# Kernel optimization log

Measured on AMD Instinct MI355X. Metric: run time of the kernel, lower is better.

Reference implementation:

```python
import jax, jax.numpy as jnp
import numpy as np

VOCAB, EMB, HID, OUT = 1000, 256, 512, 1
NUM_IN, NUM_OUT = 7, 4
B, S = 64, 512
D = EMB + NUM_OUT  # conv input dim = 260


def setup_inputs() -> dict:
    key = jax.random.key(0)
    ks = jax.random.split(key, 8)
    ev = jax.random.randint(ks[0], (B, S, 1), 0, VOCAB).astype(jnp.float32)
    num = jax.random.normal(ks[1], (B, S, NUM_IN), jnp.float32)
    X = jnp.concatenate([ev, num], axis=-1)  # [B,S,8]; col 0 = event ids
    def w(k, shape, fan_in):
        return jax.random.normal(k, shape, jnp.float32) / np.sqrt(fan_in).astype(np.float32)
    return {
        "X": X,
        "emb": w(ks[2], (VOCAB, EMB), EMB),
        "Wn": w(ks[3], (NUM_IN, NUM_OUT), NUM_IN), "bn": jnp.zeros((NUM_OUT,), jnp.float32),
        "Wf": w(ks[4], (D, 3 * HID), D), "bf": jnp.zeros((3 * HID,), jnp.float32),
        "Wb": w(ks[5], (D, 3 * HID), D), "bb": jnp.zeros((3 * HID,), jnp.float32),
        "Wo": w(ks[6], (2 * HID, OUT), 2 * HID), "bo": jnp.zeros((OUT,), jnp.float32),
    }


def _fo_pool(Z, F):
    # Z, F: [S, B, H]. Linear recurrence h_t = F_t * h_{t-1} + (1 - F_t) * Z_t.
    def step(h, zf):
        z, f = zf
        h = f * h + (1.0 - f) * z
        return h, h
    h0 = jnp.zeros(Z.shape[1:], Z.dtype)
    _, hs = jax.lax.scan(step, h0, (Z, F))
    return hs  # [S, B, H]


def _forward(X, emb, Wn, bn, Wf, bf, Wb, bb, Wo, bo):
    ev = jax.lax.stop_gradient(X[:, :, 0]).astype(jnp.int32)  # event-type ids
    num = X[:, :, 1:]
    e = emb[ev]                          # [B,S,EMB]
    n = num @ Wn + bn                    # [B,S,NUM_OUT]
    c = jnp.concatenate([e, n], axis=-1)  # [B,S,D]

    def gates(W, b):
        g = jnp.einsum('bsd,dk->sbk', c, W) + b  # kernel-1 conv == GEMM; [S,B,3H]
        Z, F = g[..., :HID], g[..., HID:2 * HID]  # O gate is computed but unused upstream
        return jnp.tanh(Z), jax.nn.sigmoid(F)

    Zf, Ff = gates(Wf, bf)
    Zb, Fb = gates(Wb, bb)
    hf = _fo_pool(Zf, Ff)                       # forward direction
    hb = _fo_pool(Zb[::-1], Fb[::-1])[::-1]     # backward: scan reversed, re-reverse
    # torch takes h_combined[-1]: last forward state, first backward-scan state
    final = jnp.concatenate([hf[-1], hb[-1]], axis=-1)  # [B, 2H]
    return final @ Wo + bo  # dropout p=0 is identity


def reference(X, emb, Wn, bn, Wf, bf, Wb, bb, Wo, bo):
    return _forward(X, emb, Wn, bn, Wf, bf, Wb, bb, Wo, bo)
```

## Files before the change

kernel.cpp:

```cpp
#include <hip/hip_runtime.h>
#include <stdint.h>

#define B_ 64
#define S_ 512
#define EMB_ 256
#define NIN_ 7
#define NOUT_ 4
#define HID_ 512
#define VOCAB_ 1000
#define VP_ 1024
#define NG_ 2048

typedef __bf16 bf16x8 __attribute__((ext_vector_type(8)));
typedef float floatx4 __attribute__((ext_vector_type(4)));
typedef unsigned short u16x8 __attribute__((ext_vector_type(8)));
typedef unsigned long long ull;

__device__ __forceinline__ unsigned short f2bf(float f) {
    unsigned u = __float_as_uint(f);
    u += 0x7FFFu + ((u >> 16) & 1u);
    return (unsigned short)(u >> 16);
}
__device__ __forceinline__ float bf2f(unsigned short h) {
    return __uint_as_float(((unsigned)h) << 16);
}
__device__ __forceinline__ float rcp_(float x) { return __builtin_amdgcn_rcpf(x); }
__device__ __forceinline__ float exp2_(float x) {
    float r; asm("v_exp_f32 %0, %1" : "=v"(r) : "v"(x)); return r;
}
#define L2E_ 1.4426950408889634f
__device__ __forceinline__ float sigmoidf_(float x) {
    return rcp_(1.0f + exp2_(x * (-L2E_)));
}
__device__ __forceinline__ float tanhf_(float x) {
    float ax = fabsf(x);
    float e = exp2_(ax * (-2.0f * L2E_));
    float t = (1.0f - e) * rcp_(1.0f + e);
    return copysignf(t, x);
}


__global__ __launch_bounds__(256) void prep(
    const float* __restrict__ emb, const float* __restrict__ bn,
    const float* __restrict__ Wf, const float* __restrict__ bfv,
    const float* __restrict__ Wb, const float* __restrict__ bb,
    unsigned short* __restrict__ Aemb, unsigned short* __restrict__ WT,
    float* __restrict__ W4, float* __restrict__ bvec,
    unsigned* __restrict__ bcnt) {
    int bid = blockIdx.x;
    int tid = threadIdx.x;

    if (bid < 64) {
        int g = bid;
#pragma unroll
        for (int half = 0; half < 2; ++half) {
            int t = tid + 256 * half;
            int r15 = t & 15;
            int kchunk = (t >> 4) & 3;
            int kt = t >> 6;
            int row = g * 16 + r15;
            int k0 = kt * 32 + kchunk * 8;
            unsigned short p[8];
            if (row < VOCAB_) {
                float4 a = *(const float4*)(emb + (size_t)row * EMB_ + k0);
                float4 b = *(const float4*)(emb + (size_t)row * EMB_ + k0 + 4);
                p[0]=f2bf(a.x); p[1]=f2bf(a.y); p[2]=f2bf(a.z); p[3]=f2bf(a.w);
                p[4]=f2bf(b.x); p[5]=f2bf(b.y); p[6]=f2bf(b.z); p[7]=f2bf(b.w);
            } else {
#pragma unroll
                for (int q = 0; q < 8; ++q) p[q] = 0;
            }
            size_t chunk = ((size_t)(g >> 3) * 8 + kt) * 8 + (g & 7);
            *(u16x8*)(Aemb + chunk * 512 + (16 * kchunk + r15) * 8) =
                *(const u16x8*)p;
        }
    } else if (bid < 192) {
        __shared__ float raw[32][132];
        int job = bid - 64;
        int idx = job >> 3;
        int kt  = job & 7;
        int p = idx >> 3;
        int gq = idx & 7;
        const float* W = p ? Wb : Wf;
        int j0 = gq * 64;
        int r = tid >> 3;
        int i = tid & 7;
        int k0 = kt * 32;

        const float* src = W + (size_t)(k0 + r) * 1536;
        float4 a0 = *(const float4*)(src + j0 + i * 8);
        float4 a1 = *(const float4*)(src + j0 + i * 8 + 4);
        float4 b0 = *(const float4*)(src + 512 + j0 + i * 8);
        float4 b1 = *(const float4*)(src + 512 + j0 + i * 8 + 4);
        *(float4*)&raw[r][i * 8]          = a0;
        *(float4*)&raw[r][i * 8 + 4]      = a1;
        *(float4*)&raw[r][64 + i * 8]     = b0;
        *(float4*)&raw[r][64 + i * 8 + 4] = b1;
        __syncthreads();
#pragma unroll
        for (int h = 0; h < 2; ++h) {
            int e = tid + 256 * h;
            int gl = e >> 6;
            int rest = e & 63;
            int kchunk = rest >> 4;
            int v15 = rest & 15;
            int joff = gl * 8 + (v15 >> 1);
            int cl = joff + 64 * (v15 & 1);
            unsigned short pk[8];
#pragma unroll
            for (int q = 0; q < 8; ++q) pk[q] = f2bf(raw[kchunk * 8 + q][cl]);
            int g = p * 64 + gq * 8 + gl;
            size_t chunk = ((size_t)(g >> 3) * 8 + kt) * 8 + (g & 7);
            *(u16x8*)(WT + chunk * 512 + (16 * kchunk + v15) * 8) =
                *(const u16x8*)pk;
        }
    } else {
        int v = (bid - 192) * 256 + tid;
        int part = v >> 10;
        int m = v & 1023;
        int j = m >> 1;
        int c = (m & 1) ? (512 + j) : j;
        const float* W = part ? Wb : Wf;
        float bv = part ? bb[c] : bfv[c];
#pragma unroll
        for (int q = 0; q < NOUT_; ++q) {
            float w = W[(size_t)(256 + q) * 1536 + c];
            W4[(size_t)q * NG_ + v] = w;
            bv = fmaf(bn[q], w, bv);
        }
        bvec[v] = bv;
        if (bid == 192 && tid < 64) bcnt[tid] = 0;
    }
}

__global__ __launch_bounds__(256) void gemmG(
    const float* __restrict__ X,
    const unsigned short* __restrict__ Aemb, const unsigned short* __restrict__ WT,
    const float* __restrict__ bvec,
    unsigned short* __restrict__ G1, unsigned short* __restrict__ Gb) {
    int bid = blockIdx.x;
    int tid = threadIdx.x;
    int lane = tid & 63, wave = tid >> 6;
    int rl = lane & 15;

    if (bid < 64) {
        int mtile = bid & 7;
        int ntile = bid >> 3;
        int r0 = mtile * 128;
        int n0 = ntile * 128;
        int wm = wave & 1, wn = wave >> 1;

        const unsigned short* pa = Aemb + ((size_t)mtile * 64 + 4 * wm) * 512 + lane * 8;
        const unsigned short* pb = WT + ((size_t)ntile * 64 + 4 * wn) * 512 + lane * 8;

        floatx4 acc[4][4];
#pragma unroll
        for (int mi = 0; mi < 4; ++mi)
#pragma unroll
            for (int ni = 0; ni < 4; ++ni) acc[mi][ni] = (floatx4){0.f, 0.f, 0.f, 0.f};

        bf16x8 afc[4], bfc[4], afn[4], bfn[4];
#pragma unroll
        for (int mi = 0; mi < 4; ++mi) afc[mi] = *(const bf16x8*)(pa + mi * 512);
#pragma unroll
        for (int ni = 0; ni < 4; ++ni) bfc[ni] = *(const bf16x8*)(pb + ni * 512);

#pragma unroll
        for (int kt = 0; kt < 8; ++kt) {
            if (kt < 7) {
#pragma unroll
                for (int mi = 0; mi < 4; ++mi)
                    afn[mi] = *(const bf16x8*)(pa + (size_t)(kt + 1) * 4096 + mi * 512);
#pragma unroll
                for (int ni = 0; ni < 4; ++ni)
                    bfn[ni] = *(const bf16x8*)(pb + (size_t)(kt + 1) * 4096 + ni * 512);
            }
#pragma unroll
            for (int mi = 0; mi < 4; ++mi)
#pragma unroll
                for (int ni = 0; ni < 4; ++ni)
                    acc[mi][ni] = __builtin_amdgcn_mfma_f32_16x16x32_bf16(afc[mi], bfc[ni], acc[mi][ni], 0, 0, 0);
            if (kt < 7) {
#pragma unroll
                for (int mi = 0; mi < 4; ++mi) afc[mi] = afn[mi];
#pragma unroll
                for (int ni = 0; ni < 4; ++ni) bfc[ni] = bfn[ni];
            }
        }

#pragma unroll
        for (int ni = 0; ni < 4; ++ni) {
            int n = n0 + 64 * wn + 16 * ni + rl;
            float bv = bvec[n];
#pragma unroll
            for (int mi = 0; mi < 4; ++mi) {
                int rb = r0 + 64 * wm + 16 * mi + (lane >> 4) * 4;
#pragma unroll
                for (int v = 0; v < 4; ++v)
                    G1[(size_t)(rb + v) * 1024 + n] = f2bf(acc[mi][ni][v] + bv);
            }
        }
    } else {
        __shared__ int evs[64];
        int ntile = bid - 64;
        int n0 = ntile * 128;
        if (tid < 64)
            evs[tid] = (int)X[((size_t)tid * S_ + (S_ - 1)) * 8];
        __syncthreads();

        int cbase[4];
#pragma unroll
        for (int mi = 0; mi < 4; ++mi) {
            int R = evs[16 * mi + rl];
            int g = R >> 4;
            cbase[mi] = (g >> 3) * 32768 + (g & 7) * 512 + (lane >> 4) * 128 + (R & 15) * 8;
        }
        const unsigned short* pb = WT + ((size_t)(8 + ntile) * 64 + 2 * wave) * 512 + lane * 8;

        floatx4 acc[4][2];
#pragma unroll
        for (int mi = 0; mi < 4; ++mi)
#pragma unroll
            for (int ni = 0; ni < 2; ++ni) acc[mi][ni] = (floatx4){0.f, 0.f, 0.f, 0.f};

#pragma unroll
        for (int kt = 0; kt < 8; ++kt) {
            bf16x8 afc[4], bfc[2];
#pragma unroll
            for (int mi = 0; mi < 4; ++mi)
                afc[mi] = *(const bf16x8*)(Aemb + (size_t)cbase[mi] + (size_t)kt * 4096);
#pragma unroll
            for (int ni = 0; ni < 2; ++ni)
                bfc[ni] = *(const bf16x8*)(pb + (size_t)kt * 4096 + ni * 512);
#pragma unroll
            for (int mi = 0; mi < 4; ++mi)
#pragma unroll
                for (int ni = 0; ni < 2; ++ni)
                    acc[mi][ni] = __builtin_amdgcn_mfma_f32_16x16x32_bf16(afc[mi], bfc[ni], acc[mi][ni], 0, 0, 0);
        }

#pragma unroll
        for (int ni = 0; ni < 2; ++ni) {
            int n = n0 + 32 * wave + 16 * ni + rl;
            float bv = bvec[1024 + n];
#pragma unroll
            for (int mi = 0; mi < 4; ++mi) {
                int rb = 16 * mi + (lane >> 4) * 4;
#pragma unroll
                for (int v = 0; v < 4; ++v)
                    Gb[(size_t)(rb + v) * 1024 + n] = f2bf(acc[mi][ni][v] + bv);
            }
        }
    }
}

__global__ __launch_bounds__(512, 4) void scanF(
    const float* __restrict__ X, const unsigned short* __restrict__ G1,
    const unsigned short* __restrict__ Gb, const float* __restrict__ W4,
    const float* __restrict__ Wn, const float* __restrict__ Wo,
    const float* __restrict__ bo, float* __restrict__ PQ,
    unsigned* __restrict__ bcnt, float* __restrict__ out) {
    __shared__ float LX[512];
    __shared__ float LN[64][4];
    __shared__ int   LO[64];
    __shared__ unsigned lastf;
    __shared__ float red[8];
    int bid = blockIdx.x;
    int b = bid >> 3, chunk = bid & 7;
    int s0 = chunk * 64;
    int j = threadIdx.x;

    LX[j] = X[((size_t)b * S_ + s0 + (j >> 3)) * 8 + (j & 7)];
    __syncthreads();

    if (j < 64) LO[j] = (int)LX[j * 8] * 2048;
    if (j < 256) {
        int t = j >> 2, q = j & 3;
        float s = 0.f;
#pragma unroll
        for (int i = 0; i < NIN_; ++i) s = fmaf(LX[t * 8 + 1 + i], Wn[i * NOUT_ + q], s);
        LN[t][q] = s;
    }

    float2 w4p[NOUT_];
#pragma unroll
    for (int q = 0; q < NOUT_; ++q)
        w4p[q] = *(const float2*)(W4 + (size_t)q * NG_ + 2 * j);
    __syncthreads();

    const char* Gbase = (const char*)G1 + 4 * j;
    unsigned gp[64];
#pragma unroll
    for (int m = 0; m < 16; ++m) {
        int4 lo = *(const int4*)&LO[4 * m];
        gp[4 * m + 0] = *(const unsigned*)(Gbase + lo.x);
        gp[4 * m + 1] = *(const unsigned*)(Gbase + lo.y);
        gp[4 * m + 2] = *(const unsigned*)(Gbase + lo.z);
        gp[4 * m + 3] = *(const unsigned*)(Gbase + lo.w);
    }

    float P = 1.f, Q = 0.f;
#pragma unroll
    for (int s = 0; s < 64; ++s) {
        unsigned gpc = gp[s];
        float gz = bf2f((unsigned short)(gpc & 0xffffu));
        float gf = bf2f((unsigned short)(gpc >> 16));
        float4 n4 = *(const float4*)(&LN[s][0]);
        gz = fmaf(n4.x, w4p[0].x, gz);
        gz = fmaf(n4.y, w4p[1].x, gz);
        gz = fmaf(n4.z, w4p[2].x, gz);
        gz = fmaf(n4.w, w4p[3].x, gz);
        gf = fmaf(n4.x, w4p[0].y, gf);
        gf = fmaf(n4.y, w4p[1].y, gf);
        gf = fmaf(n4.z, w4p[2].y, gf);
        gf = fmaf(n4.w, w4p[3].y, gf);
        float z = tanhf_(gz);
        float f = sigmoidf_(gf);
        Q = fmaf(f, Q - z, z);
        P *= f;
    }
    {
        union { float2 f; ull q; } pv;
        pv.f = make_float2(P, Q);
        __hip_atomic_store((ull*)PQ + (size_t)bid * 512 + j, pv.q,
                           __ATOMIC_RELAXED, __HIP_MEMORY_SCOPE_AGENT);
    }

    __syncthreads();
    if (j == 0) {
        unsigned old = __hip_atomic_fetch_add(bcnt + b, 1u, __ATOMIC_RELAXED,
                                              __HIP_MEMORY_SCOPE_AGENT);
        lastf = (old == 7u);
    }
    __syncthreads();

    if (lastf) {
        float h = 0.f;
#pragma unroll
        for (int c = 0; c < 8; ++c) {
            union { float2 f; ull q; } pv;
            pv.q = __hip_atomic_load((const ull*)PQ + ((size_t)b * 8 + c) * 512 + j,
                                     __ATOMIC_RELAXED, __HIP_MEMORY_SCOPE_AGENT);
            h = fmaf(pv.f.x, h, pv.f.y);
        }

        const float* xr = X + ((size_t)b * S_ + (S_ - 1)) * 8;
        float n4[NOUT_];
#pragma unroll
        for (int q = 0; q < NOUT_; ++q) {
            float s = 0.f;
#pragma unroll
            for (int i = 0; i < NIN_; ++i) s = fmaf(xr[1 + i], Wn[i * NOUT_ + q], s);
            n4[q] = s;
        }
        unsigned gpc = *(const unsigned*)(Gb + (size_t)b * 1024 + 2 * j);
        float gz = bf2f((unsigned short)(gpc & 0xffffu));
        float gf = bf2f((unsigned short)(gpc >> 16));
#pragma unroll
        for (int q = 0; q < NOUT_; ++q) {
            float2 w = *(const float2*)(W4 + (size_t)q * NG_ + 1024 + 2 * j);
            gz = fmaf(n4[q], w.x, gz);
            gf = fmaf(n4[q], w.y, gf);
        }
        float hb = (1.f - sigmoidf_(gf)) * tanhf_(gz);

        float partial = fmaf(h, Wo[j], hb * Wo[512 + j]);
#pragma unroll
        for (int off = 32; off > 0; off >>= 1)
            partial += __shfl_down(partial, off);
        if ((j & 63) == 0) red[j >> 6] = partial;
        __syncthreads();
        if (j == 0) {
            float s = bo[0];
#pragma unroll
            for (int w = 0; w < 8; ++w) s += red[w];
            out[b] = s;
        }
    }
}

extern "C" void kernel_launch(void* const* d_in, const int* in_sizes, int n_in,
                              void* d_out, int out_size, void* d_ws, size_t ws_size,
                              hipStream_t stream) {
    const float* X   = (const float*)d_in[0];
    const float* emb = (const float*)d_in[1];
    const float* Wn  = (const float*)d_in[2];
    const float* bn  = (const float*)d_in[3];
    const float* Wf  = (const float*)d_in[4];
    const float* bfv = (const float*)d_in[5];
    const float* Wb  = (const float*)d_in[6];
    const float* bb  = (const float*)d_in[7];
    const float* Wo  = (const float*)d_in[8];
    const float* bo  = (const float*)d_in[9];
    float* out = (float*)d_out;

    size_t off_A  = 0;
    size_t off_WT = off_A  + (size_t)VP_ * EMB_ * 2;
    size_t off_G1 = off_WT + (size_t)NG_ * EMB_ * 2;
    size_t off_Gb = off_G1 + (size_t)VP_ * 1024 * 2;
    size_t off_W4 = off_Gb + (size_t)B_ * 1024 * 2;
    size_t off_bv = off_W4 + (size_t)NOUT_ * NG_ * 4;
    size_t off_PQ = off_bv + (size_t)NG_ * 4;
    size_t off_bc = off_PQ + (size_t)B_ * 8 * 512 * 2 * sizeof(float);
    size_t need   = off_bc + 64 * sizeof(unsigned);
    if (ws_size < need) return;

    unsigned short* Aemb = (unsigned short*)((char*)d_ws + off_A);
    unsigned short* WT   = (unsigned short*)((char*)d_ws + off_WT);
    unsigned short* G1   = (unsigned short*)((char*)d_ws + off_G1);
    unsigned short* Gb   = (unsigned short*)((char*)d_ws + off_Gb);
    float*          W4   = (float*)((char*)d_ws + off_W4);
    float*          bvec = (float*)((char*)d_ws + off_bv);
    float*          PQ   = (float*)((char*)d_ws + off_PQ);
    unsigned*       bcnt = (unsigned*)((char*)d_ws + off_bc);

    prep<<<200, 256, 0, stream>>>(emb, bn, Wf, bfv, Wb, bb, Aemb, WT, W4, bvec, bcnt);
    gemmG<<<72, 256, 0, stream>>>(X, Aemb, WT, bvec, G1, Gb);
    scanF<<<512, 512, 0, stream>>>(X, G1, Gb, W4, Wn, Wo, bo, PQ, bcnt, out);
}
```

Measured before the change: 102.4 us.

## Fuse weight/embedding prep into GEMM kernel, dropping a launch and intermediate buffers

The separate prep kernel that converted the embedding table and gate weights to bf16 MFMA layouts is merged into the GEMM kernel. Each GEMM block now stages fp32 weight tiles through LDS, converts them on the fly, and computes the bias fold in its epilogue. This removes one kernel launch and the round trip through the Aemb/WT/bvec workspace buffers. In exchange, every block repeats the conversion work and adds per-k-step barriers. The scan kernel also hoists its W4 loads earlier and reads X with vectorized float4 loads.

After: 110.3 us. 1.08x slower.

```diff
diff --git a/kernel.cpp b/kernel.cpp
--- a/kernel.cpp
+++ b/kernel.cpp
@@ -40,209 +40,160 @@
 }
 
 
-__global__ __launch_bounds__(256) void prep(
-    const float* __restrict__ emb, const float* __restrict__ bn,
-    const float* __restrict__ Wf, const float* __restrict__ bfv,
-    const float* __restrict__ Wb, const float* __restrict__ bb,
-    unsigned short* __restrict__ Aemb, unsigned short* __restrict__ WT,
-    float* __restrict__ W4, float* __restrict__ bvec,
-    unsigned* __restrict__ bcnt) {
+__global__ __launch_bounds__(256) void gemmF(
+    const float* __restrict__ X, const float* __restrict__ emb,
+    const float* __restrict__ bn, const float* __restrict__ Wf,
+    const float* __restrict__ bfv, const float* __restrict__ Wb,
+    const float* __restrict__ bb,
+    unsigned short* __restrict__ G1, unsigned short* __restrict__ Gb,
+    float* __restrict__ W4, unsigned* __restrict__ bcnt) {
     int bid = blockIdx.x;
     int tid = threadIdx.x;
 
-    if (bid < 64) {
-        int g = bid;
-#pragma unroll
-        for (int half = 0; half < 2; ++half) {
-            int t = tid + 256 * half;
-            int r15 = t & 15;
-            int kchunk = (t >> 4) & 3;
-            int kt = t >> 6;
-            int row = g * 16 + r15;
-            int k0 = kt * 32 + kchunk * 8;
-            unsigned short p[8];
-            if (row < VOCAB_) {
+    if (bid >= 72) {
+        int v = (bid - 72) * 256 + tid;
+        int part = v >> 10;
+        int m = v & 1023;
+        int c = (m & 1) ? (512 + (m >> 1)) : (m >> 1);
+        const float* W = part ? Wb : Wf;
+#pragma unroll
+        for (int q = 0; q < NOUT_; ++q)
+            W4[(size_t)q * NG_ + v] = W[(size_t)(256 + q) * 1536 + c];
+        if (bid == 72 && tid < 64) bcnt[tid] = 0;
+        return;
+    }
+
+    __shared__ float raw[32][132];
+    __shared__ int evs[64];
+    const bool fwd = (bid < 64);
+    int mtile = fwd ? (bid & 7) : 0;
+    int ntile = fwd ? (bid >> 3) : (bid - 64);
+    const float* Wsrc = fwd ? Wf : Wb;
+    const float* bsrc = fwd ? bfv : bb;
+    int j0 = ntile * 64;
+    int lane = tid & 63, wave = tid >> 6;
+    int rl = lane & 15, kq = lane >> 4;
+    int sr = tid >> 3, si = tid & 7;
+    int wm = wave & 1, wn = wave >> 1;
+
+    float bnr[NOUT_];
+#pragma unroll
+    for (int q = 0; q < NOUT_; ++q) bnr[q] = bn[q];
+
+    if (!fwd && tid < 64)
+        evs[tid] = (int)X[((size_t)tid * S_ + (S_ - 1)) * 8];
+
+    floatx4 acc[4][4];
+#pragma unroll
+    for (int mi = 0; mi < 4; ++mi)
+#pragma unroll
+        for (int ni = 0; ni < 4; ++ni) acc[mi][ni] = (floatx4){0.f, 0.f, 0.f, 0.f};
+
+    const float* src0 = Wsrc + (size_t)sr * 1536;
+    float4 sa0 = *(const float4*)(src0 + j0 + si * 8);
+    float4 sa1 = *(const float4*)(src0 + j0 + si * 8 + 4);
+    float4 sb0 = *(const float4*)(src0 + 512 + j0 + si * 8);
+    float4 sb1 = *(const float4*)(src0 + 512 + j0 + si * 8 + 4);
+
+#pragma unroll
+    for (int kt = 0; kt < 8; ++kt) {
+        if (kt) __syncthreads();
+        *(float4*)&raw[sr][si * 8]          = sa0;
+        *(float4*)&raw[sr][si * 8 + 4]      = sa1;
+        *(float4*)&raw[sr][64 + si * 8]     = sb0;
+        *(float4*)&raw[sr][64 + si * 8 + 4] = sb1;
+        __syncthreads();
+        if (kt < 7) {
+            const float* srcn = Wsrc + (size_t)(32 * (kt + 1) + sr) * 1536;
+            sa0 = *(const float4*)(srcn + j0 + si * 8);
+            sa1 = *(const float4*)(srcn + j0 + si * 8 + 4);
+            sb0 = *(const float4*)(srcn + 512 + j0 + si * 8);
+            sb1 = *(const float4*)(srcn + 512 + j0 + si * 8 + 4);
+        }
+        int k0 = kt * 32 + kq * 8;
+
+        if (fwd) {
+            bf16x8 bf[4];
+#pragma unroll
+            for (int ni = 0; ni < 4; ++ni) {
+                int vc = wn * 64 + ni * 16 + rl;
+                int cl = (vc >> 1) + 64 * (vc & 1);
+                unsigned short pk[8];
+#pragma unroll
+                for (int q = 0; q < 8; ++q) pk[q] = f2bf(raw[kq * 8 + q][cl]);
+                bf[ni] = *(const bf16x8*)pk;
+            }
+#pragma unroll
+            for (int mi = 0; mi < 4; ++mi) {
+                int row = mtile * 128 + wm * 64 + mi * 16 + rl;
+                unsigned short pa[8];
+                if (row < VOCAB_) {
+                    float4 a = *(const float4*)(emb + (size_t)row * EMB_ + k0);
+                    float4 b = *(const float4*)(emb + (size_t)row * EMB_ + k0 + 4);
+                    pa[0]=f2bf(a.x); pa[1]=f2bf(a.y); pa[2]=f2bf(a.z); pa[3]=f2bf(a.w);
+                    pa[4]=f2bf(b.x); pa[5]=f2bf(b.y); pa[6]=f2bf(b.z); pa[7]=f2bf(b.w);
+                } else {
+#pragma unroll
+                    for (int q = 0; q < 8; ++q) pa[q] = 0;
+                }
+                bf16x8 af = *(const bf16x8*)pa;
+#pragma unroll
+                for (int ni = 0; ni < 4; ++ni)
+                    acc[mi][ni] = __builtin_amdgcn_mfma_f32_16x16x32_bf16(af, bf[ni], acc[mi][ni], 0, 0, 0);
+            }
+        } else {
+            bf16x8 bf[2];
+#pragma unroll
+            for (int ni = 0; ni < 2; ++ni) {
+                int vc = wave * 32 + ni * 16 + rl;
+                int cl = (vc >> 1) + 64 * (vc & 1);
+                unsigned short pk[8];
+#pragma unroll
+                for (int q = 0; q < 8; ++q) pk[q] = f2bf(raw[kq * 8 + q][cl]);
+                bf[ni] = *(const bf16x8*)pk;
+            }
+#pragma unroll
+            for (int mi = 0; mi < 4; ++mi) {
+                int row = evs[16 * mi + rl];
                 float4 a = *(const float4*)(emb + (size_t)row * EMB_ + k0);
                 float4 b = *(const float4*)(emb + (size_t)row * EMB_ + k0 + 4);
-                p[0]=f2bf(a.x); p[1]=f2bf(a.y); p[2]=f2bf(a.z); p[3]=f2bf(a.w);
-                p[4]=f2bf(b.x); p[5]=f2bf(b.y); p[6]=f2bf(b.z); p[7]=f2bf(b.w);
-            } else {
-#pragma unroll
-                for (int q = 0; q < 8; ++q) p[q] = 0;
-            }
-            size_t chunk = ((size_t)(g >> 3) * 8 + kt) * 8 + (g & 7);
-            *(u16x8*)(Aemb + chunk * 512 + (16 * kchunk + r15) * 8) =
-                *(const u16x8*)p;
-        }
-    } else if (bid < 192) {
-        __shared__ float raw[32][132];
-        int job = bid - 64;
-        int idx = job >> 3;
-        int kt  = job & 7;
-        int p = idx >> 3;
-        int gq = idx & 7;
-        const float* W = p ? Wb : Wf;
-        int j0 = gq * 64;
-        int r = tid >> 3;
-        int i = tid & 7;
-        int k0 = kt * 32;
-
-        const float* src = W + (size_t)(k0 + r) * 1536;
-        float4 a0 = *(const float4*)(src + j0 + i * 8);
-        float4 a1 = *(const float4*)(src + j0 + i * 8 + 4);
-        float4 b0 = *(const float4*)(src + 512 + j0 + i * 8);
-        float4 b1 = *(const float4*)(src + 512 + j0 + i * 8 + 4);
-        *(float4*)&raw[r][i * 8]          = a0;
-        *(float4*)&raw[r][i * 8 + 4]      = a1;
-        *(float4*)&raw[r][64 + i * 8]     = b0;
-        *(float4*)&raw[r][64 + i * 8 + 4] = b1;
-        __syncthreads();
-#pragma unroll
-        for (int h = 0; h < 2; ++h) {
-            int e = tid + 256 * h;
-            int gl = e >> 6;
-            int rest = e & 63;
-            int kchunk = rest >> 4;
-            int v15 = rest & 15;
-            int joff = gl * 8 + (v15 >> 1);
-            int cl = joff + 64 * (v15 & 1);
-            unsigned short pk[8];
-#pragma unroll
-            for (int q = 0; q < 8; ++q) pk[q] = f2bf(raw[kchunk * 8 + q][cl]);
-            int g = p * 64 + gq * 8 + gl;
-            size_t chunk = ((size_t)(g >> 3) * 8 + kt) * 8 + (g & 7);
-            *(u16x8*)(WT + chunk * 512 + (16 * kchunk + v15) * 8) =
-                *(const u16x8*)pk;
-        }
-    } else {
-        int v = (bid - 192) * 256 + tid;
-        int part = v >> 10;
-        int m = v & 1023;
-        int j = m >> 1;
-        int c = (m & 1) ? (512 + j) : j;
-        const float* W = part ? Wb : Wf;
-        float bv = part ? bb[c] : bfv[c];
-#pragma unroll
-        for (int q = 0; q < NOUT_; ++q) {
-            float w = W[(size_t)(256 + q) * 1536 + c];
-            W4[(size_t)q * NG_ + v] = w;
-            bv = fmaf(bn[q], w, bv);
-        }
-        bvec[v] = bv;
-        if (bid == 192 && tid < 64) bcnt[tid] = 0;
-    }
-}
-
-__global__ __launch_bounds__(256) void gemmG(
-    const float* __restrict__ X,
-    const unsigned short* __restrict__ Aemb, const unsigned short* __restrict__ WT,
-    const float* __restrict__ bvec,
-    unsigned short* __restrict__ G1, unsigned short* __restrict__ Gb) {
-    int bid = blockIdx.x;
-    int tid = threadIdx.x;
-    int lane = tid & 63, wave = tid >> 6;
-    int rl = lane & 15;
-
-    if (bid < 64) {
-        int mtile = bid & 7;
-        int ntile = bid >> 3;
-        int r0 = mtile * 128;
-        int n0 = ntile * 128;
-        int wm = wave & 1, wn = wave >> 1;
-
-        const unsigned short* pa = Aemb + ((size_t)mtile * 64 + 4 * wm) * 512 + lane * 8;
-        const unsigned short* pb = WT + ((size_t)ntile * 64 + 4 * wn) * 512 + lane * 8;
-
-        floatx4 acc[4][4];
-#pragma unroll
-        for (int mi = 0; mi < 4; ++mi)
-#pragma unroll
-            for (int ni = 0; ni < 4; ++ni) acc[mi][ni] = (floatx4){0.f, 0.f, 0.f, 0.f};
-
-        bf16x8 afc[4], bfc[4], afn[4], bfn[4];
-#pragma unroll
-        for (int mi = 0; mi < 4; ++mi) afc[mi] = *(const bf16x8*)(pa + mi * 512);
-#pragma unroll
-        for (int ni = 0; ni < 4; ++ni) bfc[ni] = *(const bf16x8*)(pb + ni * 512);
-
-#pragma unroll
-        for (int kt = 0; kt < 8; ++kt) {
-            if (kt < 7) {
-#pragma unroll
-                for (int mi = 0; mi < 4; ++mi)
-                    afn[mi] = *(const bf16x8*)(pa + (size_t)(kt + 1) * 4096 + mi * 512);
-#pragma unroll
-                for (int ni = 0; ni < 4; ++ni)
-                    bfn[ni] = *(const bf16x8*)(pb + (size_t)(kt + 1) * 4096 + ni * 512);
-            }
-#pragma unroll
-            for (int mi = 0; mi < 4; ++mi)
-#pragma unroll
-                for (int ni = 0; ni < 4; ++ni)
-                    acc[mi][ni] = __builtin_amdgcn_mfma_f32_16x16x32_bf16(afc[mi], bfc[ni], acc[mi][ni], 0, 0, 0);
-            if (kt < 7) {
-#pragma unroll
-                for (int mi = 0; mi < 4; ++mi) afc[mi] = afn[mi];
-#pragma unroll
-                for (int ni = 0; ni < 4; ++ni) bfc[ni] = bfn[ni];
-            }
-        }
-
+                unsigned short pa[8];
+                pa[0]=f2bf(a.x); pa[1]=f2bf(a.y); pa[2]=f2bf(a.z); pa[3]=f2bf(a.w);
+                pa[4]=f2bf(b.x); pa[5]=f2bf(b.y); pa[6]=f2bf(b.z); pa[7]=f2bf(b.w);
+                bf16x8 af = *(const bf16x8*)pa;
+#pragma unroll
+                for (int ni = 0; ni < 2; ++ni)
+                    acc[mi][ni] = __builtin_amdgcn_mfma_f32_16x16x32_bf16(af, bf[ni], acc[mi][ni], 0, 0, 0);
+            }
+        }
+    }
+
+    if (fwd) {
 #pragma unroll
         for (int ni = 0; ni < 4; ++ni) {
-            int n = n0 + 64 * wn + 16 * ni + rl;
-            float bv = bvec[n];
+            int n = ntile * 128 + 64 * wn + 16 * ni + rl;
+            int c = (n & 1) ? (512 + (n >> 1)) : (n >> 1);
+            float bv = bsrc[c];
+#pragma unroll
+            for (int q = 0; q < NOUT_; ++q)
+                bv = fmaf(bnr[q], Wsrc[(size_t)(256 + q) * 1536 + c], bv);
 #pragma unroll
             for (int mi = 0; mi < 4; ++mi) {
-                int rb = r0 + 64 * wm + 16 * mi + (lane >> 4) * 4;
+                int rb = mtile * 128 + 64 * wm + 16 * mi + (lane >> 4) * 4;
 #pragma unroll
                 for (int v = 0; v < 4; ++v)
                     G1[(size_t)(rb + v) * 1024 + n] = f2bf(acc[mi][ni][v] + bv);
             }
         }
     } else {
-        __shared__ int evs[64];
-        int ntile = bid - 64;
-        int n0 = ntile * 128;
-        if (tid < 64)
-            evs[tid] = (int)X[((size_t)tid * S_ + (S_ - 1)) * 8];
-        __syncthreads();
-
-        int cbase[4];
-#pragma unroll
-        for (int mi = 0; mi < 4; ++mi) {
-            int R = evs[16 * mi + rl];
-            int g = R >> 4;
-            cbase[mi] = (g >> 3) * 32768 + (g & 7) * 512 + (lane >> 4) * 128 + (R & 15) * 8;
-        }
-        const unsigned short* pb = WT + ((size_t)(8 + ntile) * 64 + 2 * wave) * 512 + lane * 8;
-
-        floatx4 acc[4][2];
-#pragma unroll
-        for (int mi = 0; mi < 4; ++mi)
-#pragma unroll
-            for (int ni = 0; ni < 2; ++ni) acc[mi][ni] = (floatx4){0.f, 0.f, 0.f, 0.f};
-
-#pragma unroll
-        for (int kt = 0; kt < 8; ++kt) {
-            bf16x8 afc[4], bfc[2];
-#pragma unroll
-            for (int mi = 0; mi < 4; ++mi)
-                afc[mi] = *(const bf16x8*)(Aemb + (size_t)cbase[mi] + (size_t)kt * 4096);
-#pragma unroll
-            for (int ni = 0; ni < 2; ++ni)
-                bfc[ni] = *(const bf16x8*)(pb + (size_t)kt * 4096 + ni * 512);
-#pragma unroll
-            for (int mi = 0; mi < 4; ++mi)
-#pragma unroll
-                for (int ni = 0; ni < 2; ++ni)
-                    acc[mi][ni] = __builtin_amdgcn_mfma_f32_16x16x32_bf16(afc[mi], bfc[ni], acc[mi][ni], 0, 0, 0);
-        }
-
 #pragma unroll
         for (int ni = 0; ni < 2; ++ni) {
-            int n = n0 + 32 * wave + 16 * ni + rl;
-            float bv = bvec[1024 + n];
+            int n = ntile * 128 + 32 * wave + 16 * ni + rl;
+            int c = (n & 1) ? (512 + (n >> 1)) : (n >> 1);
+            float bv = bsrc[c];
+#pragma unroll
+            for (int q = 0; q < NOUT_; ++q)
+                bv = fmaf(bnr[q], Wsrc[(size_t)(256 + q) * 1536 + c], bv);
 #pragma unroll
             for (int mi = 0; mi < 4; ++mi) {
                 int rb = 16 * mi + (lane >> 4) * 4;
@@ -270,7 +221,15 @@
     int s0 = chunk * 64;
     int j = threadIdx.x;
 
-    LX[j] = X[((size_t)b * S_ + s0 + (j >> 3)) * 8 + (j & 7)];
+    float2 w4p[NOUT_];
+#pragma unroll
+    for (int q = 0; q < NOUT_; ++q)
+        w4p[q] = *(const float2*)(W4 + (size_t)q * NG_ + 2 * j);
+
+    if (j < 128) {
+        const float* xb = X + ((size_t)b * S_ + s0) * 8;
+        *(float4*)&LX[4 * j] = *(const float4*)(xb + 4 * j);
+    }
     __syncthreads();
 
     if (j < 64) LO[j] = (int)LX[j * 8] * 2048;
@@ -281,11 +240,6 @@
         for (int i = 0; i < NIN_; ++i) s = fmaf(LX[t * 8 + 1 + i], Wn[i * NOUT_ + q], s);
         LN[t][q] = s;
     }
-
-    float2 w4p[NOUT_];
-#pragma unroll
-    for (int q = 0; q < NOUT_; ++q)
-        w4p[q] = *(const float2*)(W4 + (size_t)q * NG_ + 2 * j);
     __syncthreads();
 
     const char* Gbase = (const char*)G1 + 4 * j;
@@ -394,27 +348,20 @@
     const float* bo  = (const float*)d_in[9];
     float* out = (float*)d_out;
 
-    size_t off_A  = 0;
-    size_t off_WT = off_A  + (size_t)VP_ * EMB_ * 2;
-    size_t off_G1 = off_WT + (size_t)NG_ * EMB_ * 2;
+    size_t off_G1 = 0;
     size_t off_Gb = off_G1 + (size_t)VP_ * 1024 * 2;
     size_t off_W4 = off_Gb + (size_t)B_ * 1024 * 2;
-    size_t off_bv = off_W4 + (size_t)NOUT_ * NG_ * 4;
-    size_t off_PQ = off_bv + (size_t)NG_ * 4;
+    size_t off_PQ = off_W4 + (size_t)NOUT_ * NG_ * 4;
     size_t off_bc = off_PQ + (size_t)B_ * 8 * 512 * 2 * sizeof(float);
     size_t need   = off_bc + 64 * sizeof(unsigned);
     if (ws_size < need) return;
 
-    unsigned short* Aemb = (unsigned short*)((char*)d_ws + off_A);
-    unsigned short* WT   = (unsigned short*)((char*)d_ws + off_WT);
     unsigned short* G1   = (unsigned short*)((char*)d_ws + off_G1);
     unsigned short* Gb   = (unsigned short*)((char*)d_ws + off_Gb);
     float*          W4   = (float*)((char*)d_ws + off_W4);
-    float*          bvec = (float*)((char*)d_ws + off_bv);
     float*          PQ   = (float*)((char*)d_ws + off_PQ);
     unsigned*       bcnt = (unsigned*)((char*)d_ws + off_bc);
 
-    prep<<<200, 256, 0, stream>>>(emb, bn, Wf, bfv, Wb, bb, Aemb, WT, W4, bvec, bcnt);
-    gemmG<<<72, 256, 0, stream>>>(X, Aemb, WT, bvec, G1, Gb);
+    gemmF<<<80, 256, 0, stream>>>(X, emb, bn, Wf, bfv, Wb, bb, G1, Gb, W4, bcnt);
     scanF<<<512, 512, 0, stream>>>(X, G1, Gb, W4, Wn, Wo, bo, PQ, bcnt, out);
 }
```
